# Kernel tuning notes

Hardware: AMD Instinct MI355X
Metric: run time of the kernel (lower is better)

The kernel has to match this reference:

```python
import jax, jax.numpy as jnp
import numpy as np

EPS = 1e-8  # torch F.cosine_similarity default eps
NEG = -1e9  # masked_fill value


def setup_inputs() -> dict:
    key = jax.random.key(0)
    k1, k2, k3 = jax.random.split(key, 3)
    B, Sq, Sk, D = 4, 2048, 2048, 1024
    query = jax.random.normal(k1, (B, Sq, 1, D), dtype=jnp.float32)
    key_t = jax.random.normal(k2, (B, 1, Sk, D), dtype=jnp.float32)
    mask = jax.random.randint(k3, (B, Sk), 0, 2, dtype=jnp.int32)
    return {"query": query, "key": key_t, "mask": mask}


def reference(query, key, mask):
    # query: [B, Sq, 1, D], key: [B, 1, Sk, D]
    q = query[:, :, 0, :]  # [B, Sq, D]
    k = key[:, 0, :, :]    # [B, Sk, D]
    # cosine_similarity(q, k, dim=3) = (q.k) / (max(|q|,eps) * max(|k|,eps))
    qn = jnp.maximum(jnp.linalg.norm(q, axis=-1), EPS)  # [B, Sq]
    kn = jnp.maximum(jnp.linalg.norm(k, axis=-1), EPS)  # [B, Sk]
    dot = jnp.einsum('bqd,bkd->bqk', q, k)              # [B, Sq, Sk]
    scores = dot / (qn[:, :, None] * kn[:, None, :])
    # mask.unsqueeze(1).repeat(1, Sq, 1) -> broadcast [B, 1, Sk] over Sq
    scores = jnp.where(mask[:, None, :] == 0, NEG, scores)
    return scores
```

## Files before the change

kernel.cpp:

```cpp
#include <hip/hip_runtime.h>
#include <hip/hip_bf16.h>
#include <stdint.h>


constexpr int B_  = 4;
constexpr int SQ  = 2048;
constexpr int SK  = 2048;
constexpr int D_  = 1024;

constexpr int BM  = 128;
constexpr int BN  = 128;

constexpr int BM2 = 256;
constexpr int BN2 = 256;
constexpr int BK2 = 32;
constexpr int NT2 = D_ / BK2;
constexpr int BUFSH     = BM2 * BK2;
constexpr int BUFSTRIDE = 2 * BUFSH;

typedef __attribute__((ext_vector_type(8)))  short    short8;
typedef __attribute__((ext_vector_type(4)))  float    f32x4;
typedef __attribute__((ext_vector_type(16))) float    f32x16;
typedef __attribute__((ext_vector_type(4)))  unsigned uint4v;
typedef unsigned int u32;

__device__ inline unsigned pack_bf16(float lo, float hi) {
  union { float f; unsigned u; } a, b;
  a.f = lo; b.f = hi;
  return __builtin_amdgcn_perm(b.u, a.u, 0x07060302u);
}

__device__ inline void async_ld16(const void* g, void* l) {
  __builtin_amdgcn_global_load_lds((const __attribute__((address_space(1))) u32*)g,
                                   (__attribute__((address_space(3))) u32*)l, 16, 0, 0);
}

constexpr int ROWS_Q = B_ * SQ;
constexpr int ROWS_T = B_ * (SQ + SK);

__global__ __launch_bounds__(256) void convert_norm(
    const float* __restrict__ Q, const float* __restrict__ Km,
    unsigned short* __restrict__ Qb, unsigned short* __restrict__ Kb,
    float* __restrict__ invQ, float* __restrict__ invK)
{
  const int row  = blockIdx.x * 4 + (threadIdx.x >> 6);
  const int lane = threadIdx.x & 63;

  const float* src; unsigned short* dst; float* inv;
  if (row < ROWS_Q) {
    src = Q  + (size_t)row * D_;
    dst = Qb + (size_t)row * D_;
    inv = invQ + row;
  } else {
    int r = row - ROWS_Q;
    src = Km + (size_t)r * D_;
    dst = Kb + (size_t)r * D_;
    inv = invK + r;
  }

  const f32x4* s4 = (const f32x4*)(src + lane * 16);
  f32x4 v[4];
  #pragma unroll
  for (int i = 0; i < 4; ++i) v[i] = s4[i];

  float ss = 0.0f;
  unsigned p[8];
  #pragma unroll
  for (int i = 0; i < 4; ++i) {
    p[2*i]   = pack_bf16(v[i].x, v[i].y);
    p[2*i+1] = pack_bf16(v[i].z, v[i].w);
    ss += v[i].x*v[i].x + v[i].y*v[i].y + v[i].z*v[i].z + v[i].w*v[i].w;
  }
  uint4v w0 = {p[0], p[1], p[2], p[3]};
  uint4v w1 = {p[4], p[5], p[6], p[7]};
  uint4v* d4 = (uint4v*)(dst + lane * 16);
  d4[0] = w0; d4[1] = w1;

  #pragma unroll
  for (int off = 32; off > 0; off >>= 1) ss += __shfl_xor(ss, off);
  if (lane == 0) *inv = 1.0f / fmaxf(sqrtf(ss), 1e-8f);
}

__global__ __launch_bounds__(512, 2) void ca_gemm_bf(
    const unsigned short* __restrict__ Qb,
    const unsigned short* __restrict__ Kb,
    const float* __restrict__ invQ,
    const float* __restrict__ invK,
    const int*   __restrict__ mask,
    float*       __restrict__ out)
{
  __shared__ __align__(16) unsigned short lds[3 * BUFSTRIDE];

  const int tid  = threadIdx.x;
  const int lane = tid & 63;
  const int w    = tid >> 6;
  const int wr   = w >> 2;
  const int wc   = w & 3;
  const int b    = blockIdx.z;
  const int tm0  = blockIdx.y * BM2;
  const int tn0  = blockIdx.x * BN2;

  const int g = (lane & 3) ^ ((lane >> 3) & 3);
  const char* qsrc = (const char*)(Qb + ((size_t)b * SQ + tm0 + w * 32 + (lane >> 2)) * D_) + g * 16;
  const char* ksrc = (const char*)(Kb + ((size_t)b * SK + tn0 + w * 32 + (lane >> 2)) * D_) + g * 16;
  const size_t RSTEP16 = (size_t)16 * D_ * 2;

  f32x16 acc[4][2];
  #pragma unroll
  for (int m = 0; m < 4; ++m)
    #pragma unroll
    for (int n = 0; n < 2; ++n)
      #pragma unroll
      for (int r = 0; r < 16; ++r) acc[m][n][r] = 0.0f;

  const int ln = lane & 31;
  const int h  = lane >> 5;
  const int qz = (ln >> 1) & 3;

  auto stage = [&](int bufw) {
    unsigned short* ba = lds + bufw * BUFSTRIDE + w * 1024;
    unsigned short* bb = ba + BUFSH;
    async_ld16(qsrc,           ba);
    async_ld16(qsrc + RSTEP16, ba + 16 * 32);
    async_ld16(ksrc,           bb);
    async_ld16(ksrc + RSTEP16, bb + 16 * 32);
    qsrc += BK2 * 2;
    ksrc += BK2 * 2;
  };

  auto compute = [&](int bufr) {
    const unsigned short* Ab = lds + bufr * BUFSTRIDE + (wr * 128 + ln) * 32;
    const unsigned short* Bb = lds + bufr * BUFSTRIDE + BUFSH + (wc * 64 + ln) * 32;
    #pragma unroll
    for (int s = 0; s < 2; ++s) {
      const int p8 = ((2 * s + h) ^ qz) * 8;
      short8 a0 = *(const short8*)(Ab + p8);
      short8 a1 = *(const short8*)(Ab + p8 + 1024);
      short8 a2 = *(const short8*)(Ab + p8 + 2048);
      short8 a3 = *(const short8*)(Ab + p8 + 3072);
      short8 b0 = *(const short8*)(Bb + p8);
      short8 b1 = *(const short8*)(Bb + p8 + 1024);
      acc[0][0] = __builtin_amdgcn_mfma_f32_32x32x16_bf16(a0, b0, acc[0][0], 0, 0, 0);
      acc[0][1] = __builtin_amdgcn_mfma_f32_32x32x16_bf16(a0, b1, acc[0][1], 0, 0, 0);
      acc[1][0] = __builtin_amdgcn_mfma_f32_32x32x16_bf16(a1, b0, acc[1][0], 0, 0, 0);
      acc[1][1] = __builtin_amdgcn_mfma_f32_32x32x16_bf16(a1, b1, acc[1][1], 0, 0, 0);
      acc[2][0] = __builtin_amdgcn_mfma_f32_32x32x16_bf16(a2, b0, acc[2][0], 0, 0, 0);
      acc[2][1] = __builtin_amdgcn_mfma_f32_32x32x16_bf16(a2, b1, acc[2][1], 0, 0, 0);
      acc[3][0] = __builtin_amdgcn_mfma_f32_32x32x16_bf16(a3, b0, acc[3][0], 0, 0, 0);
      acc[3][1] = __builtin_amdgcn_mfma_f32_32x32x16_bf16(a3, b1, acc[3][1], 0, 0, 0);
    }
  };

  stage(0);
  stage(1);
  asm volatile("s_waitcnt vmcnt(4)" ::: "memory");
  __builtin_amdgcn_s_barrier();

  int bufr = 0, bufw = 2;
  for (int t = 0; t < NT2; ++t) {
    if (t < NT2 - 2) {
      stage(bufw);
      bufw = (bufw == 2) ? 0 : bufw + 1;
    }
    compute(bufr);
    bufr = (bufr == 2) ? 0 : bufr + 1;
    if (t < NT2 - 1) {
      if (t < NT2 - 2) asm volatile("s_waitcnt vmcnt(4)" ::: "memory");
      else             asm volatile("s_waitcnt vmcnt(0)" ::: "memory");
      __builtin_amdgcn_s_barrier();
    }
  }

  #pragma unroll
  for (int n = 0; n < 2; ++n) {
    const int gc = tn0 + wc * 64 + n * 32 + ln;
    const int mk = mask[b * SK + gc];
    const float ibv = invK[b * SK + gc];
    #pragma unroll
    for (int m = 0; m < 4; ++m) {
      #pragma unroll
      for (int reg = 0; reg < 16; ++reg) {
        const int row = wr * 128 + m * 32 + (reg & 3) + 8 * (reg >> 2) + 4 * h;
        const float iav = invQ[b * SQ + tm0 + row];
        float v = mk ? acc[m][n][reg] * iav * ibv : -1000000000.0f;
        out[((size_t)b * SQ + tm0 + row) * SK + gc] = v;
      }
    }
  }
}

constexpr int LDK = 40;

__global__ __launch_bounds__(256, 2) void ca_gemm(
    const float* __restrict__ Q, const float* __restrict__ Km,
    const int* __restrict__ mask, float* __restrict__ out)
{
  __shared__ __align__(16) short As[BM * LDK];
  __shared__ __align__(16) short Bs[BN * LDK];
  __shared__ float ssA_part[256];
  __shared__ float ssB_part[256];
  __shared__ float invA[BM];
  __shared__ float invB[BN];

  const int tid  = threadIdx.x;
  const int lane = tid & 63;
  const int w    = tid >> 6;
  const int b    = blockIdx.z;
  const int tm0  = blockIdx.y * BM;
  const int tn0  = blockIdx.x * BN;

  const int ra = tid >> 1;
  const int ka = (tid & 1) * 16;

  const float* qp = Q  + ((size_t)b * SQ + tm0 + ra) * D_ + ka;
  const float* kp = Km + ((size_t)b * SK + tn0 + ra) * D_ + ka;

  f32x4 zero4 = {0.0f, 0.0f, 0.0f, 0.0f};
  f32x4 acc[4][4];
  #pragma unroll
  for (int i = 0; i < 4; ++i)
    #pragma unroll
    for (int j = 0; j < 4; ++j) acc[i][j] = zero4;

  float ssA = 0.0f, ssB = 0.0f;

  const int wm = (w >> 1) * 64;
  const int wn = (w & 1) * 64;
  const int lr = lane & 15;
  const int lq = lane >> 4;

  short* aw = &As[ra * LDK + ka];
  short* bw = &Bs[ra * LDK + ka];

  for (int k0 = 0; k0 < D_; k0 += 32) {
    f32x4 av[4], bv[4];
    #pragma unroll
    for (int i = 0; i < 4; ++i) av[i] = *(const f32x4*)(qp + 4 * i);
    #pragma unroll
    for (int i = 0; i < 4; ++i) bv[i] = *(const f32x4*)(kp + 4 * i);
    qp += 32; kp += 32;

    unsigned pa[8], pb[8];
    #pragma unroll
    for (int i = 0; i < 4; ++i) {
      pa[2*i]   = pack_bf16(av[i].x, av[i].y);
      pa[2*i+1] = pack_bf16(av[i].z, av[i].w);
      pb[2*i]   = pack_bf16(bv[i].x, bv[i].y);
      pb[2*i+1] = pack_bf16(bv[i].z, bv[i].w);
      ssA += av[i].x*av[i].x + av[i].y*av[i].y + av[i].z*av[i].z + av[i].w*av[i].w;
      ssB += bv[i].x*bv[i].x + bv[i].y*bv[i].y + bv[i].z*bv[i].z + bv[i].w*bv[i].w;
    }

    __syncthreads();
    {
      uint4v wa0 = {pa[0], pa[1], pa[2], pa[3]};
      uint4v wa1 = {pa[4], pa[5], pa[6], pa[7]};
      uint4v wb0 = {pb[0], pb[1], pb[2], pb[3]};
      uint4v wb1 = {pb[4], pb[5], pb[6], pb[7]};
      *(uint4v*)(aw)     = wa0;
      *(uint4v*)(aw + 8) = wa1;
      *(uint4v*)(bw)     = wb0;
      *(uint4v*)(bw + 8) = wb1;
    }
    __syncthreads();

    short8 af[4], bf[4];
    #pragma unroll
    for (int t = 0; t < 4; ++t)
      af[t] = *(const short8*)&As[(wm + t * 16 + lr) * LDK + lq * 8];
    #pragma unroll
    for (int t = 0; t < 4; ++t)
      bf[t] = *(const short8*)&Bs[(wn + t * 16 + lr) * LDK + lq * 8];

    #pragma unroll
    for (int i = 0; i < 4; ++i)
      #pragma unroll
      for (int j = 0; j < 4; ++j)
        acc[i][j] = __builtin_amdgcn_mfma_f32_16x16x32_bf16(af[i], bf[j], acc[i][j], 0, 0, 0);
  }

  ssA_part[tid] = ssA;
  ssB_part[tid] = ssB;
  __syncthreads();
  if (tid < BM) {
    float s = ssA_part[2 * tid] + ssA_part[2 * tid + 1];
    invA[tid] = 1.0f / fmaxf(sqrtf(s), 1e-8f);
  } else {
    int r = tid - BM;
    float s = ssB_part[2 * r] + ssB_part[2 * r + 1];
    invB[r] = 1.0f / fmaxf(sqrtf(s), 1e-8f);
  }
  __syncthreads();

  #pragma unroll
  for (int tn = 0; tn < 4; ++tn) {
    const int lc = wn + tn * 16 + lr;
    const int gc = tn0 + lc;
    const int mk = mask[b * SK + gc];
    const float ibv = invB[lc];
    #pragma unroll
    for (int tm = 0; tm < 4; ++tm) {
      const int lrow = wm + tm * 16 + lq * 4;
      #pragma unroll
      for (int r = 0; r < 4; ++r) {
        float v = mk ? acc[tm][tn][r] * invA[lrow + r] * ibv : -1000000000.0f;
        out[((size_t)b * SQ + tm0 + lrow + r) * SK + gc] = v;
      }
    }
  }
}

extern "C" void kernel_launch(void* const* d_in, const int* in_sizes, int n_in,
                              void* d_out, int out_size, void* d_ws, size_t ws_size,
                              hipStream_t stream) {
  const float* Q    = (const float*)d_in[0];
  const float* Km   = (const float*)d_in[1];
  const int*   mask = (const int*)d_in[2];
  float*       out  = (float*)d_out;

  const size_t nQ   = (size_t)B_ * SQ * D_;
  const size_t nK   = (size_t)B_ * SK * D_;
  const size_t need = (nQ + nK) * 2 + (size_t)B_ * (SQ + SK) * 4;
  if (ws_size >= need) {
    unsigned short* Qb = (unsigned short*)d_ws;
    unsigned short* Kb = Qb + nQ;
    float*          iQ = (float*)(Kb + nK);
    float*          iK = iQ + (size_t)B_ * SQ;
    convert_norm<<<ROWS_T / 4, 256, 0, stream>>>(Q, Km, Qb, Kb, iQ, iK);
    dim3 grid(SK / BN2, SQ / BM2, B_);
    ca_gemm_bf<<<grid, dim3(512), 0, stream>>>(Qb, Kb, iQ, iK, mask, out);
  } else {
    dim3 grid(SK / BN, SQ / BM, B_);
    ca_gemm<<<grid, dim3(256), 0, stream>>>(Q, Km, mask, out);
  }
}
```

Measured before the change: 162.6 us.

## Deepen LDS pipeline to four stages with split A/B prefetch and ping-pong barriers

Moves from a 3-buffer to a 4-buffer LDS ring with a prefetch distance of three K-tiles. The A and B tile loads are issued separately between the two MFMA half-steps. Each MFMA cluster is bracketed by barriers and s_setprio so the waves stay in lockstep and MFMA issue gets priority. The goal is to hide global-to-LDS latency and smooth memory/compute interleaving, at the cost of more LDS per block (which may cut occupancy at 2 blocks per CU) and extra barriers per iteration.

```diff
diff --git a/kernel.cpp b/kernel.cpp
--- a/kernel.cpp
+++ b/kernel.cpp
@@ -15,8 +15,8 @@
 constexpr int BN2 = 256;
 constexpr int BK2 = 32;
 constexpr int NT2 = D_ / BK2;
-constexpr int BUFSH     = BM2 * BK2;
-constexpr int BUFSTRIDE = 2 * BUFSH;
+constexpr int ATS = BM2 * BK2;
+constexpr int BUFSH = 2 * ATS;
 
 typedef __attribute__((ext_vector_type(8)))  short    short8;
 typedef __attribute__((ext_vector_type(4)))  float    f32x4;
@@ -89,7 +89,7 @@
     const int*   __restrict__ mask,
     float*       __restrict__ out)
 {
-  __shared__ __align__(16) unsigned short lds[3 * BUFSTRIDE];
+  __shared__ __align__(16) unsigned short lds[4 * BUFSH];
 
   const int tid  = threadIdx.x;
   const int lane = tid & 63;
@@ -100,10 +100,11 @@
   const int tm0  = blockIdx.y * BM2;
   const int tn0  = blockIdx.x * BN2;
 
-  const int g = (lane & 3) ^ ((lane >> 3) & 3);
-  const char* qsrc = (const char*)(Qb + ((size_t)b * SQ + tm0 + w * 32 + (lane >> 2)) * D_) + g * 16;
-  const char* ksrc = (const char*)(Kb + ((size_t)b * SK + tn0 + w * 32 + (lane >> 2)) * D_) + g * 16;
-  const size_t RSTEP16 = (size_t)16 * D_ * 2;
+  const int g = (tid & 3) ^ ((tid >> 3) & 3);
+  const char* qs = (const char*)(Qb + ((size_t)b * SQ + tm0 + (tid >> 2)) * D_) + g * 16;
+  const char* ks = (const char*)(Kb + ((size_t)b * SK + tn0 + (tid >> 2)) * D_) + g * 16;
+  const size_t HALFB = (size_t)128 * D_ * 2;
+  unsigned short* dst0 = lds + tid * 8;
 
   f32x16 acc[4][2];
   #pragma unroll
@@ -117,29 +118,42 @@
   const int h  = lane >> 5;
   const int qz = (ln >> 1) & 3;
 
-  auto stage = [&](int bufw) {
-    unsigned short* ba = lds + bufw * BUFSTRIDE + w * 1024;
-    unsigned short* bb = ba + BUFSH;
-    async_ld16(qsrc,           ba);
-    async_ld16(qsrc + RSTEP16, ba + 16 * 32);
-    async_ld16(ksrc,           bb);
-    async_ld16(ksrc + RSTEP16, bb + 16 * 32);
-    qsrc += BK2 * 2;
-    ksrc += BK2 * 2;
+  auto stageA = [&](int t) {
+    unsigned short* base = dst0 + (t & 3) * BUFSH;
+    const char* s = qs + (size_t)t * (BK2 * 2);
+    async_ld16(s,         base);
+    async_ld16(s + HALFB, base + ATS / 2);
   };
-
-  auto compute = [&](int bufr) {
-    const unsigned short* Ab = lds + bufr * BUFSTRIDE + (wr * 128 + ln) * 32;
-    const unsigned short* Bb = lds + bufr * BUFSTRIDE + BUFSH + (wc * 64 + ln) * 32;
-    #pragma unroll
-    for (int s = 0; s < 2; ++s) {
-      const int p8 = ((2 * s + h) ^ qz) * 8;
+  auto stageB = [&](int t) {
+    unsigned short* base = dst0 + (t & 3) * BUFSH + ATS;
+    const char* s = ks + (size_t)t * (BK2 * 2);
+    async_ld16(s,         base);
+    async_ld16(s + HALFB, base + ATS / 2);
+  };
+
+  stageA(0); stageB(0);
+  stageA(1); stageB(1);
+  stageA(2); stageB(2);
+  asm volatile("s_waitcnt vmcnt(8)" ::: "memory");
+  __builtin_amdgcn_s_barrier();
+
+  for (int t = 0; t < NT2; ++t) {
+    const unsigned short* Ab = lds + (t & 3) * BUFSH + (wr * 128 + ln) * 32;
+    const unsigned short* Bb = lds + (t & 3) * BUFSH + ATS + (wc * 64 + ln) * 32;
+    const bool pre = (t + 3 < NT2);
+
+    {
+      const int p8 = (h ^ qz) * 8;
       short8 a0 = *(const short8*)(Ab + p8);
       short8 a1 = *(const short8*)(Ab + p8 + 1024);
       short8 a2 = *(const short8*)(Ab + p8 + 2048);
       short8 a3 = *(const short8*)(Ab + p8 + 3072);
       short8 b0 = *(const short8*)(Bb + p8);
       short8 b1 = *(const short8*)(Bb + p8 + 1024);
+      if (pre) stageA(t + 3);
+      __builtin_amdgcn_sched_barrier(0);
+      __builtin_amdgcn_s_barrier();
+      __builtin_amdgcn_s_setprio(1);
       acc[0][0] = __builtin_amdgcn_mfma_f32_32x32x16_bf16(a0, b0, acc[0][0], 0, 0, 0);
       acc[0][1] = __builtin_amdgcn_mfma_f32_32x32x16_bf16(a0, b1, acc[0][1], 0, 0, 0);
       acc[1][0] = __builtin_amdgcn_mfma_f32_32x32x16_bf16(a1, b0, acc[1][0], 0, 0, 0);
@@ -148,25 +162,35 @@
       acc[2][1] = __builtin_amdgcn_mfma_f32_32x32x16_bf16(a2, b1, acc[2][1], 0, 0, 0);
       acc[3][0] = __builtin_amdgcn_mfma_f32_32x32x16_bf16(a3, b0, acc[3][0], 0, 0, 0);
       acc[3][1] = __builtin_amdgcn_mfma_f32_32x32x16_bf16(a3, b1, acc[3][1], 0, 0, 0);
-    }
-  };
-
-  stage(0);
-  stage(1);
-  asm volatile("s_waitcnt vmcnt(4)" ::: "memory");
-  __builtin_amdgcn_s_barrier();
-
-  int bufr = 0, bufw = 2;
-  for (int t = 0; t < NT2; ++t) {
-    if (t < NT2 - 2) {
-      stage(bufw);
-      bufw = (bufw == 2) ? 0 : bufw + 1;
-    }
-    compute(bufr);
-    bufr = (bufr == 2) ? 0 : bufr + 1;
-    if (t < NT2 - 1) {
-      if (t < NT2 - 2) asm volatile("s_waitcnt vmcnt(4)" ::: "memory");
-      else             asm volatile("s_waitcnt vmcnt(0)" ::: "memory");
+      __builtin_amdgcn_s_setprio(0);
+      __builtin_amdgcn_s_barrier();
+    }
+
+    {
+      const int p8 = ((2 + h) ^ qz) * 8;
+      short8 a0 = *(const short8*)(Ab + p8);
+      short8 a1 = *(const short8*)(Ab + p8 + 1024);
+      short8 a2 = *(const short8*)(Ab + p8 + 2048);
+      short8 a3 = *(const short8*)(Ab + p8 + 3072);
+      short8 b0 = *(const short8*)(Bb + p8);
+      short8 b1 = *(const short8*)(Bb + p8 + 1024);
+      if (pre) stageB(t + 3);
+      __builtin_amdgcn_sched_barrier(0);
+      __builtin_amdgcn_s_barrier();
+      __builtin_amdgcn_s_setprio(1);
+      acc[0][0] = __builtin_amdgcn_mfma_f32_32x32x16_bf16(a0, b0, acc[0][0], 0, 0, 0);
+      acc[0][1] = __builtin_amdgcn_mfma_f32_32x32x16_bf16(a0, b1, acc[0][1], 0, 0, 0);
+      acc[1][0] = __builtin_amdgcn_mfma_f32_32x32x16_bf16(a1, b0, acc[1][0], 0, 0, 0);
+      acc[1][1] = __builtin_amdgcn_mfma_f32_32x32x16_bf16(a1, b1, acc[1][1], 0, 0, 0);
+      acc[2][0] = __builtin_amdgcn_mfma_f32_32x32x16_bf16(a2, b0, acc[2][0], 0, 0, 0);
+      acc[2][1] = __builtin_amdgcn_mfma_f32_32x32x16_bf16(a2, b1, acc[2][1], 0, 0, 0);
+      acc[3][0] = __builtin_amdgcn_mfma_f32_32x32x16_bf16(a3, b0, acc[3][0], 0, 0, 0);
+      acc[3][1] = __builtin_amdgcn_mfma_f32_32x32x16_bf16(a3, b1, acc[3][1], 0, 0, 0);
+      __builtin_amdgcn_s_setprio(0);
+      if (t < NT2 - 1) {
+        if (t < NT2 - 3) asm volatile("s_waitcnt vmcnt(8)" ::: "memory");
+        else             asm volatile("s_waitcnt vmcnt(0)" ::: "memory");
+      }
       __builtin_amdgcn_s_barrier();
     }
   }
```

After: 165.6 us. About the same (+1.8%).
